# Performance work log

Hardware: AMD Instinct MI355X
Metric: run time of the kernel (lower is better)

The kernel has to match this reference:

```python
import jax, jax.numpy as jnp
import numpy as np

D_MODEL = 1024
N_HEADS = 16
D_H = D_MODEL // N_HEADS
MAX_LEN = 2048
BATCH = 2
SEQ = 2048
EPS = 1e-8
W_SCALE = 0.02


def _rms_norm(x, w):
    # RMSNorm: x * rsqrt(mean(x^2) + eps) * w
    ms = jnp.mean(jnp.square(x), axis=-1, keepdims=True)
    return w * (x * jax.lax.rsqrt(ms + EPS))


def setup_inputs() -> dict:
    key = jax.random.key(0)
    ks = jax.random.split(key, 12)
    d = D_MODEL
    inp = {
        "x": jax.random.normal(ks[0], (BATCH, SEQ, d), dtype=jnp.float32),
        "t_bias": jnp.zeros((1,), dtype=jnp.float32),  # unused by the module
        "p_bias": jax.random.normal(ks[1], (MAX_LEN, N_HEADS), dtype=jnp.float32),
        # AMS layer params (Linear stored as [in, out])
        "wq": jax.random.normal(ks[2], (d, d), dtype=jnp.float32) * W_SCALE,
        "bq": jnp.zeros((d,), dtype=jnp.float32),
        "wk": jax.random.normal(ks[3], (d, d), dtype=jnp.float32) * W_SCALE,
        "bk": jnp.zeros((d,), dtype=jnp.float32),
        "wv": jax.random.normal(ks[4], (d, d), dtype=jnp.float32) * W_SCALE,
        "bv": jnp.zeros((d,), dtype=jnp.float32),
        "wu": jax.random.normal(ks[5], (d, d), dtype=jnp.float32) * W_SCALE,
        "bu": jnp.zeros((d,), dtype=jnp.float32),
        "g_ams": jnp.ones((d,), dtype=jnp.float32),   # shared RMSNorm weight in AMSLayer
        # MFFN layer params
        "w0": jax.random.normal(ks[6], (d, d), dtype=jnp.float32) * W_SCALE,
        "b0": jnp.zeros((d,), dtype=jnp.float32),
        "w1": jax.random.normal(ks[7], (d, 2 * d), dtype=jnp.float32) * W_SCALE,
        "b1": jnp.zeros((2 * d,), dtype=jnp.float32),
        "w2": jax.random.normal(ks[8], (d, d), dtype=jnp.float32) * W_SCALE,
        "b2": jnp.zeros((d,), dtype=jnp.float32),
        "g_mffn": jnp.ones((d,), dtype=jnp.float32),
    }
    return inp


def reference(x, t_bias, p_bias, wq, bq, wk, bk, wv, bv, wu, bu, g_ams,
              w0, b0, w1, b1, w2, b2, g_mffn):
    B, S, d = x.shape
    H, dh = N_HEADS, D_H

    # ---- AMS layer ----
    x_norm = _rms_norm(x, g_ams)

    def proj(w, b):
        # [B,S,d] -> [B,H,S,dh]
        return (x_norm @ w + b).reshape(B, S, H, dh).transpose(0, 2, 1, 3)

    q = proj(wq, bq)
    k = proj(wk, bk)
    v = proj(wv, bv)

    scale = 1.0 / np.sqrt(dh).astype(np.float32)
    score = jnp.einsum('bhsd,bhtd->bhst', q, k) * scale
    # additive positional bias: p_bias[:S].T -> [H,S], broadcast over query dim
    score = score + p_bias[:S, :].T[None, :, None, :]

    attn = jax.nn.silu(score)                        # SiLU instead of softmax
    out = jnp.einsum('bhst,bhtd->bhsd', attn, v)
    out = out.transpose(0, 2, 1, 3).reshape(B, S, d)

    u = jax.nn.silu(x_norm @ wu + bu)
    ams_out = _rms_norm(out, g_ams) * u

    # ---- MFFN layer ----
    o = (ams_out @ w0 + b0) + x
    o_norm = _rms_norm(o, g_mffn)
    x12 = o_norm @ w1 + b1
    x1, x2 = jnp.split(x12, 2, axis=-1)
    swiglu = jax.nn.silu(x1) * x2
    return (swiglu @ w2 + b2) + o
```

## Files before the change

kernel.cpp:

```cpp
#include <hip/hip_runtime.h>
#include <stdint.h>
#include <math.h>


#define D    1024
#define NH   16
#define DH   64
#define B_   2
#define S_   2048
#define ROWS 4096
#define LQ   4096
#define EPSR 1e-8f

typedef unsigned short u16;
typedef __attribute__((ext_vector_type(8))) short short8;
typedef __attribute__((ext_vector_type(4))) float f32x4;

__device__ __forceinline__ float bf2f(u16 u) {
    union { uint32_t i; float f; } c; c.i = ((uint32_t)u) << 16; return c.f;
}
__device__ __forceinline__ u16 f2bf(float f) {
    union { float f; uint32_t i; } c; c.f = f;
    uint32_t x = c.i;
    x += 0x7fffu + ((x >> 16) & 1u);
    return (u16)(x >> 16);
}
__device__ __forceinline__ uint32_t pack2bf(float a, float b) {
    union { float f; uint32_t i; } ca, cb; ca.f = a; cb.f = b;
    return __builtin_amdgcn_perm(cb.i + 0x8000u, ca.i + 0x8000u, 0x07060302);
}
#define LOG2E 1.44269504f
__device__ __forceinline__ float silu_fast(float v) {
    return v * __builtin_amdgcn_rcpf(1.0f + __builtin_amdgcn_exp2f(v * -LOG2E));
}

__global__ __launch_bounds__(256) void transpose_all_kernel(
    const float* __restrict__ wq, const float* __restrict__ wk,
    const float* __restrict__ wv, const float* __restrict__ wu,
    const float* __restrict__ w0, const float* __restrict__ w2,
    const float* __restrict__ w1,
    u16* __restrict__ wT4, u16* __restrict__ w0T,
    u16* __restrict__ w2T, u16* __restrict__ w1T)
{
    const unsigned MI = 1u << 20;
    const int z = blockIdx.z;
    const float* W; u16* WT; int N; int noff = 0;
    switch (z) {
        case 0: W = wq; WT = wT4;          N = 1024; break;
        case 1: W = wk; WT = wT4 + 1 * MI; N = 1024; break;
        case 2: W = wv; WT = wT4 + 2 * MI; N = 1024; break;
        case 3: W = wu; WT = wT4 + 3 * MI; N = 1024; break;
        case 4: W = w0; WT = w0T;          N = 1024; break;
        case 5: W = w2; WT = w2T;          N = 1024; break;
        case 6: W = w1; WT = w1T;          N = 2048; noff = 0;    break;
        default:W = w1; WT = w1T;          N = 2048; noff = 1024; break;
    }
    __shared__ float T[64][65];
    const int tid = threadIdx.x;
    const int n0 = (blockIdx.x << 6) + noff;
    const int k0 = blockIdx.y << 6;
    const int rr = tid >> 4;
    const int cc = (tid & 15) << 2;
#pragma unroll
    for (int l = 0; l < 4; ++l) {
        const int r = rr + (l << 4);
        float4 v = *(const float4*)&W[(size_t)(k0 + r) * N + n0 + cc];
        T[cc + 0][r] = v.x; T[cc + 1][r] = v.y;
        T[cc + 2][r] = v.z; T[cc + 3][r] = v.w;
    }
    __syncthreads();
    const int n  = tid >> 2;
    const int ks = (tid & 3) << 4;
#pragma unroll
    for (int m = 0; m < 4; ++m) {
        const int k = ks + (m << 2);
        float4 v = *(const float4*)&T[n][k];
        ushort4 o;
        o.x = f2bf(v.x); o.y = f2bf(v.y); o.z = f2bf(v.z); o.w = f2bf(v.w);
        *(ushort4*)&WT[(size_t)(n0 + n) * 1024 + k0 + k] = o;
    }
}

__global__ __launch_bounds__(256) void pbt_kernel(
    const float* __restrict__ pb, float* __restrict__ pbT)
{
    const int tid = threadIdx.x;
    const int r = (blockIdx.x << 7) + (tid >> 1);
    const int c0 = (tid & 1) << 3;
    float4 v0 = *(const float4*)&pb[(size_t)r * NH + c0];
    float4 v1 = *(const float4*)&pb[(size_t)r * NH + c0 + 4];
    pbT[(size_t)(c0 + 0) * S_ + r] = v0.x;
    pbT[(size_t)(c0 + 1) * S_ + r] = v0.y;
    pbT[(size_t)(c0 + 2) * S_ + r] = v0.z;
    pbT[(size_t)(c0 + 3) * S_ + r] = v0.w;
    pbT[(size_t)(c0 + 4) * S_ + r] = v1.x;
    pbT[(size_t)(c0 + 5) * S_ + r] = v1.y;
    pbT[(size_t)(c0 + 6) * S_ + r] = v1.z;
    pbT[(size_t)(c0 + 7) * S_ + r] = v1.w;
}

__global__ __launch_bounds__(256) void rmsnorm_kernel(
    const float* __restrict__ inf, const u16* __restrict__ inb, int ldi,
    const float* __restrict__ g,
    const u16* __restrict__ mul, int ldm,
    u16* __restrict__ out, int ldo)
{
    const int row = blockIdx.x;
    const int tid = threadIdx.x;
    const int c = tid << 2;
    float x0, x1, x2, x3;
    if (inb) {
        ushort4 xi = *(const ushort4*)&inb[(size_t)row * ldi + c];
        x0 = bf2f(xi.x); x1 = bf2f(xi.y); x2 = bf2f(xi.z); x3 = bf2f(xi.w);
    } else {
        float4 xi = *(const float4*)&inf[(size_t)row * ldi + c];
        x0 = xi.x; x1 = xi.y; x2 = xi.z; x3 = xi.w;
    }
    float ss = x0*x0 + x1*x1 + x2*x2 + x3*x3;
#pragma unroll
    for (int off = 32; off > 0; off >>= 1) ss += __shfl_down(ss, off, 64);
    __shared__ float red[4];
    if ((tid & 63) == 0) red[tid >> 6] = ss;
    __syncthreads();
    float r = rsqrtf((red[0] + red[1] + red[2] + red[3]) * (1.0f / D) + EPSR);
    float4 gv = *(const float4*)&g[c];
    float v0 = x0 * r * gv.x, v1 = x1 * r * gv.y, v2 = x2 * r * gv.z, v3 = x3 * r * gv.w;
    if (mul) {
        ushort4 mi = *(const ushort4*)&mul[(size_t)row * ldm + c];
        v0 *= bf2f(mi.x); v1 *= bf2f(mi.y); v2 *= bf2f(mi.z); v3 *= bf2f(mi.w);
    }
    ushort4 o;
    o.x = f2bf(v0); o.y = f2bf(v1); o.z = f2bf(v2); o.w = f2bf(v3);
    *(ushort4*)&out[(size_t)row * ldo + c] = o;
}

__global__ __launch_bounds__(256) void gemm128(
    const u16* __restrict__ A, const u16* __restrict__ WT,
    const float* __restrict__ bs0, const float* __restrict__ bs1,
    const float* __restrict__ bs2, const float* __restrict__ bs3,
    u16* __restrict__ outb, int ldo, int actmask,
    u16* __restrict__ VT, int vtsel)
{
    __shared__ u16 As[128 * 32];
    __shared__ u16 Bs[128 * 32];
    const int tid  = threadIdx.x;
    const int wave = tid >> 6;
    const int lane = tid & 63;
    const int lm   = lane & 15;
    const int quad = lane >> 4;
    const int row0 = blockIdx.y << 7;
    const int col0 = blockIdx.x << 7;
    const int wr = (wave >> 1) << 6;
    const int wc = (wave & 1) << 6;

    const int srow = wave * 32 + (lane >> 2);
    const int skp  = (lane & 3) << 3;
    const u16* Ag = A  + (size_t)(row0 + srow) * 1024 + skp;
    const u16* Bg = WT + (size_t)(col0 + srow) * 1024 + skp;
    u16* Asd0 = &As[(wave * 32) * 32];
    u16* Asd1 = &As[(wave * 32 + 16) * 32];
    u16* Bsd0 = &Bs[(wave * 32) * 32];
    u16* Bsd1 = &Bs[(wave * 32 + 16) * 32];

    f32x4 acc[4][4] = {};

    for (int k0 = 0; k0 < 1024; k0 += 32) {
        __syncthreads();
        __builtin_amdgcn_global_load_lds(
            (const __attribute__((address_space(1))) void*)(Ag + k0),
            (__attribute__((address_space(3))) void*)Asd0, 16, 0, 0);
        __builtin_amdgcn_global_load_lds(
            (const __attribute__((address_space(1))) void*)(Ag + 16 * 1024 + k0),
            (__attribute__((address_space(3))) void*)Asd1, 16, 0, 0);
        __builtin_amdgcn_global_load_lds(
            (const __attribute__((address_space(1))) void*)(Bg + k0),
            (__attribute__((address_space(3))) void*)Bsd0, 16, 0, 0);
        __builtin_amdgcn_global_load_lds(
            (const __attribute__((address_space(1))) void*)(Bg + 16 * 1024 + k0),
            (__attribute__((address_space(3))) void*)Bsd1, 16, 0, 0);
        __syncthreads();
        short8 af[4], bf[4];
#pragma unroll
        for (int i = 0; i < 4; ++i)
            af[i] = *(const short8*)&As[(wr + i * 16 + lm) * 32 + quad * 8];
#pragma unroll
        for (int j = 0; j < 4; ++j)
            bf[j] = *(const short8*)&Bs[(wc + j * 16 + lm) * 32 + quad * 8];
#pragma unroll
        for (int i = 0; i < 4; ++i)
#pragma unroll
            for (int j = 0; j < 4; ++j)
                acc[i][j] = __builtin_amdgcn_mfma_f32_16x16x32_bf16(af[i], bf[j], acc[i][j], 0, 0, 0);
    }
    const int sel = col0 >> 10;
    const float* bias = (sel == 0) ? bs0 : (sel == 1) ? bs1 : (sel == 2) ? bs2 : bs3;
    const int act = (actmask >> sel) & 1;
    if (VT && sel == vtsel) {
        const int b = row0 >> 11;
#pragma unroll
        for (int j = 0; j < 4; ++j) {
            const int c2 = (col0 + wc + j * 16 + lm) & 1023;
            const int h  = c2 >> 6;
            const int dh = c2 & 63;
            const float bj = bias[c2];
            u16* vrow = VT + ((size_t)(b * NH + h) * 64 + dh) * (size_t)S_;
#pragma unroll
            for (int i = 0; i < 4; ++i) {
                const int tb = (row0 & 2047) + wr + i * 16 + quad * 4;
                ushort4 o;
                o.x = f2bf(acc[i][j][0] + bj);
                o.y = f2bf(acc[i][j][1] + bj);
                o.z = f2bf(acc[i][j][2] + bj);
                o.w = f2bf(acc[i][j][3] + bj);
                *(ushort4*)&vrow[tb] = o;
            }
        }
    } else {
#pragma unroll
        for (int j = 0; j < 4; ++j) {
            const int colg = col0 + wc + j * 16 + lm;
            const float bj = bias[colg & 1023];
#pragma unroll
            for (int i = 0; i < 4; ++i) {
#pragma unroll
                for (int r = 0; r < 4; ++r) {
                    const int rowg = row0 + wr + i * 16 + quad * 4 + r;
                    float v = acc[i][j][r] + bj;
                    if (act) v = silu_fast(v);
                    outb[(size_t)rowg * ldo + colg] = f2bf(v);
                }
            }
        }
    }
}

__global__ __launch_bounds__(256) void gemm64(
    const u16* __restrict__ A, int lda, const u16* __restrict__ WT,
    const float* __restrict__ bias,
    const float* __restrict__ res,
    float* __restrict__ outf, int ldo)
{
    __shared__ u16 As[128 * 32];
    __shared__ u16 Bs[64 * 32];
    const int tid  = threadIdx.x;
    const int wave = tid >> 6;
    const int lane = tid & 63;
    const int lm   = lane & 15;
    const int quad = lane >> 4;
    const int row0 = blockIdx.y << 7;
    const int col0 = blockIdx.x << 6;
    const int wr = (wave >> 1) << 6;
    const int wc = (wave & 1) << 5;

    const int srA = wave * 32 + (lane >> 2);
    const int srB = wave * 16 + (lane >> 2);
    const int skp = (lane & 3) << 3;
    const u16* Ag = A  + (size_t)(row0 + srA) * lda + skp;
    const u16* Bg = WT + (size_t)(col0 + srB) * 1024 + skp;
    u16* Asd0 = &As[(wave * 32) * 32];
    u16* Asd1 = &As[(wave * 32 + 16) * 32];
    u16* Bsd  = &Bs[(wave * 16) * 32];

    f32x4 acc[4][2] = {};

    for (int k0 = 0; k0 < 1024; k0 += 32) {
        __syncthreads();
        __builtin_amdgcn_global_load_lds(
            (const __attribute__((address_space(1))) void*)(Ag + k0),
            (__attribute__((address_space(3))) void*)Asd0, 16, 0, 0);
        __builtin_amdgcn_global_load_lds(
            (const __attribute__((address_space(1))) void*)(Ag + (size_t)16 * lda + k0),
            (__attribute__((address_space(3))) void*)Asd1, 16, 0, 0);
        __builtin_amdgcn_global_load_lds(
            (const __attribute__((address_space(1))) void*)(Bg + k0),
            (__attribute__((address_space(3))) void*)Bsd, 16, 0, 0);
        __syncthreads();
        short8 af[4], bf[2];
#pragma unroll
        for (int i = 0; i < 4; ++i)
            af[i] = *(const short8*)&As[(wr + i * 16 + lm) * 32 + quad * 8];
#pragma unroll
        for (int j = 0; j < 2; ++j)
            bf[j] = *(const short8*)&Bs[(wc + j * 16 + lm) * 32 + quad * 8];
#pragma unroll
        for (int i = 0; i < 4; ++i)
#pragma unroll
            for (int j = 0; j < 2; ++j)
                acc[i][j] = __builtin_amdgcn_mfma_f32_16x16x32_bf16(af[i], bf[j], acc[i][j], 0, 0, 0);
    }
#pragma unroll
    for (int j = 0; j < 2; ++j) {
        const int colg = col0 + wc + j * 16 + lm;
        const float bj = bias[colg];
#pragma unroll
        for (int i = 0; i < 4; ++i) {
#pragma unroll
            for (int r = 0; r < 4; ++r) {
                const int rowg = row0 + wr + i * 16 + quad * 4 + r;
                const size_t idx = (size_t)rowg * ldo + colg;
                float v = acc[i][j][r] + bj;
                if (res) v += res[idx];
                outf[idx] = v;
            }
        }
    }
}

__global__ __launch_bounds__(256, 4) void attn_mfma(
    const u16* __restrict__ qkvu, const u16* __restrict__ VT,
    const float* __restrict__ pbT, u16* __restrict__ out)
{
    __shared__ u16 Ks[2][64 * 64];
    __shared__ u16 Vs[2][64 * 64];
    const int tid  = threadIdx.x;
    const int wave = tid >> 6;
    const int lane = tid & 63;
    const int lm   = lane & 15;
    const int quad = lane >> 4;
    const int flat = blockIdx.x + (blockIdx.y << 5) + (blockIdx.z << 9);
    const int work = ((flat & 7) << 7) + (flat >> 3);
    const int s0 = (work & 31) << 6;
    const int h  = (work >> 5) & 15;
    const int b  = work >> 9;
    const size_t base = (size_t)b * S_ * LQ + (size_t)h * DH;
    const u16* q  = qkvu + base;
    const u16* kg = qkvu + base + 1024;
    const u16* vt = VT + (size_t)(b * NH + h) * 64 * S_;
    const float* pbh = pbT + (size_t)h * S_;

    short8 qf[2];
#pragma unroll
    for (int kk = 0; kk < 2; ++kk)
        qf[kk] = *(const short8*)&q[(size_t)(s0 + wave * 16 + lm) * LQ + kk * 32 + quad * 8];

    const int lr  = lane >> 3;
    const int gch = (lane & 7) ^ lr;
    const u16* kg0 = kg + (size_t)(16 * wave + lr) * LQ + gch * 8;
    const u16* vg0 = vt + (size_t)(16 * wave + lr) * S_ + gch * 8;
    const int cof0 = ((0 * 4 + quad) ^ (lm & 7)) * 8;
    const int cof1 = ((1 * 4 + quad) ^ (lm & 7)) * 8;
    const int a0   = (lm + ((quad & 1) << 5)) << 2;
    const bool hi  = quad >= 2;

#define GLDS(gp, lp) __builtin_amdgcn_global_load_lds( \
        (const __attribute__((address_space(1))) void*)(gp), \
        (__attribute__((address_space(3))) void*)(lp), 16, 0, 0)

    GLDS(kg0,                     &Ks[0][(16 * wave) * 64]);
    GLDS(kg0 + (size_t)8 * LQ,    &Ks[0][(16 * wave + 8) * 64]);
    GLDS(vg0,                     &Vs[0][(16 * wave) * 64]);
    GLDS(vg0 + (size_t)8 * S_,    &Vs[0][(16 * wave + 8) * 64]);

    f32x4 accO[4] = {};
    __syncthreads();

    for (int t0 = 0; t0 < S_; t0 += 64) {
        const int ib = (t0 >> 6) & 1;
        const int nb = ib ^ 1;
        float4 pbv[4];
#pragma unroll
        for (int mt = 0; mt < 4; ++mt)
            pbv[mt] = *(const float4*)&pbh[t0 + mt * 16 + quad * 4];
        if (t0 + 64 < S_) {
            const size_t tn = (size_t)(t0 + 64);
            GLDS(kg0 + tn * LQ,             &Ks[nb][(16 * wave) * 64]);
            GLDS(kg0 + (tn + 8) * LQ,       &Ks[nb][(16 * wave + 8) * 64]);
            GLDS(vg0 + tn,                  &Vs[nb][(16 * wave) * 64]);
            GLDS(vg0 + tn + (size_t)8 * S_, &Vs[nb][(16 * wave + 8) * 64]);
        }
        short8 kf[4][2];
#pragma unroll
        for (int mt = 0; mt < 4; ++mt) {
            kf[mt][0] = *(const short8*)&Ks[ib][(mt * 16 + lm) * 64 + cof0];
            kf[mt][1] = *(const short8*)&Ks[ib][(mt * 16 + lm) * 64 + cof1];
        }
        f32x4 st[4] = {};
#pragma unroll
        for (int mt = 0; mt < 4; ++mt)
#pragma unroll
            for (int kk = 0; kk < 2; ++kk)
                st[mt] = __builtin_amdgcn_mfma_f32_16x16x32_bf16(kf[mt][kk], qf[kk], st[mt], 0, 0, 0);
        int stp[4][2];
#pragma unroll
        for (int mt = 0; mt < 4; ++mt) {
            const float pbr[4] = {pbv[mt].x, pbv[mt].y, pbv[mt].z, pbv[mt].w};
            float p[4];
#pragma unroll
            for (int r = 0; r < 4; ++r) {
                const float a = fmaf(st[mt][r], 0.125f, pbr[r]);
                const float e = __builtin_amdgcn_exp2f(a * -LOG2E);
                p[r] = a * __builtin_amdgcn_rcpf(1.0f + e);
            }
            stp[mt][0] = (int)pack2bf(p[0], p[1]);
            stp[mt][1] = (int)pack2bf(p[2], p[3]);
        }
        short8 pf[2];
#pragma unroll
        for (int kk = 0; kk < 2; ++kk) {
            const int e0 = stp[2 * kk][0],     e1 = stp[2 * kk][1];
            const int o0 = stp[2 * kk + 1][0], o1 = stp[2 * kk + 1][1];
            const int w0a = __builtin_amdgcn_ds_bpermute(a0,      e0);
            const int w0b = __builtin_amdgcn_ds_bpermute(a0,      o0);
            const int w1a = __builtin_amdgcn_ds_bpermute(a0,      e1);
            const int w1b = __builtin_amdgcn_ds_bpermute(a0,      o1);
            const int w2a = __builtin_amdgcn_ds_bpermute(a0 + 64, e0);
            const int w2b = __builtin_amdgcn_ds_bpermute(a0 + 64, o0);
            const int w3a = __builtin_amdgcn_ds_bpermute(a0 + 64, e1);
            const int w3b = __builtin_amdgcn_ds_bpermute(a0 + 64, o1);
            int4 pw;
            pw.x = hi ? w0b : w0a;
            pw.y = hi ? w1b : w1a;
            pw.z = hi ? w2b : w2a;
            pw.w = hi ? w3b : w3a;
            pf[kk] = *(const short8*)&pw;
        }
        short8 vf[4][2];
#pragma unroll
        for (int nj = 0; nj < 4; ++nj) {
            vf[nj][0] = *(const short8*)&Vs[ib][(nj * 16 + lm) * 64 + cof0];
            vf[nj][1] = *(const short8*)&Vs[ib][(nj * 16 + lm) * 64 + cof1];
        }
#pragma unroll
        for (int nj = 0; nj < 4; ++nj)
#pragma unroll
            for (int kk = 0; kk < 2; ++kk)
                accO[nj] = __builtin_amdgcn_mfma_f32_16x16x32_bf16(pf[kk], vf[nj][kk], accO[nj], 0, 0, 0);
        __syncthreads();
    }
#undef GLDS
    const int srow = s0 + wave * 16 + quad * 4;
#pragma unroll
    for (int nj = 0; nj < 4; ++nj)
#pragma unroll
        for (int r = 0; r < 4; ++r)
            out[base + (size_t)(srow + r) * LQ + nj * 16 + lm] = f2bf(accO[nj][r]);
}

__global__ __launch_bounds__(256) void swiglu_kernel(u16* __restrict__ qkvu)
{
    const size_t e = ((size_t)blockIdx.x * 256 + threadIdx.x) << 2;
    const size_t r = e >> 10;
    const int    c = (int)(e & 1023);
    ushort4 a = *(const ushort4*)&qkvu[r * LQ + c];
    ushort4 b = *(const ushort4*)&qkvu[r * LQ + 1024 + c];
    ushort4 o;
    o.x = f2bf(silu_fast(bf2f(a.x)) * bf2f(b.x));
    o.y = f2bf(silu_fast(bf2f(a.y)) * bf2f(b.y));
    o.z = f2bf(silu_fast(bf2f(a.z)) * bf2f(b.z));
    o.w = f2bf(silu_fast(bf2f(a.w)) * bf2f(b.w));
    *(ushort4*)&qkvu[r * LQ + 2048 + c] = o;
}

extern "C" void kernel_launch(void* const* d_in, const int* in_sizes, int n_in,
                              void* d_out, int out_size, void* d_ws, size_t ws_size,
                              hipStream_t stream)
{
    const float* x      = (const float*)d_in[0];
    const float* pb     = (const float*)d_in[2];
    const float* wq     = (const float*)d_in[3];
    const float* bq     = (const float*)d_in[4];
    const float* wk     = (const float*)d_in[5];
    const float* bk     = (const float*)d_in[6];
    const float* wv     = (const float*)d_in[7];
    const float* bv     = (const float*)d_in[8];
    const float* wu     = (const float*)d_in[9];
    const float* bu     = (const float*)d_in[10];
    const float* g_ams  = (const float*)d_in[11];
    const float* w0     = (const float*)d_in[12];
    const float* b0     = (const float*)d_in[13];
    const float* w1     = (const float*)d_in[14];
    const float* b1     = (const float*)d_in[15];
    const float* w2     = (const float*)d_in[16];
    const float* b2     = (const float*)d_in[17];
    const float* g_mffn = (const float*)d_in[18];
    float* OUT = (float*)d_out;
    u16*   VT  = (u16*)d_out;
    float* pbT = (float*)((u16*)d_out + 4 * (1u << 20));

    const size_t MI = 1024 * 1024;
    u16* WS   = (u16*)d_ws;
    u16* wT4  = WS;
    u16* w0T  = WS + 4 * MI;
    u16* w2T  = WS + 5 * MI;
    u16* w1T  = WS + 6 * MI;
    u16* A0   = WS + 8 * MI;
    u16* QKVU = WS + 12 * MI;

    dim3 blk(256);

    transpose_all_kernel<<<dim3(16, 16, 8), blk, 0, stream>>>(
        wq, wk, wv, wu, w0, w2, w1, wT4, w0T, w2T, w1T);
    pbt_kernel<<<16, blk, 0, stream>>>(pb, pbT);

    rmsnorm_kernel<<<ROWS, blk, 0, stream>>>(x, nullptr, D, g_ams, nullptr, 0, A0, D);
    gemm128<<<dim3(32, 32), blk, 0, stream>>>(A0, wT4, bq, bk, bv, bu,
                                              QKVU, LQ, 0b1000, VT, 2);
    attn_mfma<<<dim3(32, 16, 2), blk, 0, stream>>>(QKVU, VT, pbT, QKVU);
    rmsnorm_kernel<<<ROWS, blk, 0, stream>>>(nullptr, QKVU, LQ, g_ams, QKVU + 3072, LQ, A0, D);
    gemm64<<<dim3(16, 32), blk, 0, stream>>>(A0, D, w0T, b0, x, OUT, D);
    rmsnorm_kernel<<<ROWS, blk, 0, stream>>>(OUT, nullptr, D, g_mffn, nullptr, 0, A0, D);
    gemm128<<<dim3(16, 32), blk, 0, stream>>>(A0, w1T, b1, b1 + 1024, b1, b1,
                                              QKVU, LQ, 0, nullptr, -1);
    swiglu_kernel<<<ROWS * D / 1024, blk, 0, stream>>>(QKVU);
    gemm64<<<dim3(16, 32), blk, 0, stream>>>(QKVU + 2048, LQ, w2T, b2, OUT, OUT, D);
    (void)ws_size; (void)in_sizes; (void)n_in; (void)out_size;
}
```

Measured before the change: 352.9 us.

## Rewrite attention with 32x32x16 MFMA, 128-row query tiles and permlane swap

The attention kernel moves from 16x16x32 to 32x32x16 bf16 MFMA tiles, with each wave owning 32 query rows and each block 128 rows, which halves the grid. The score-to-operand shuffle now uses v_permlane32_swap instead of eight ds_bpermute calls, packing uses v_cvt_pk_bf16_f32, and the positional bias is staged once into LDS rather than loaded from global every iteration. s_setprio hints are placed around the MFMA sections. The aim is to cut LDS and permute traffic and raise MFMA efficiency, at the cost of more accumulator registers per thread and fewer blocks, which may reduce occupancy.

New measurement: 343.8 us. 2.6% less time.

```diff
diff --git a/kernel.cpp b/kernel.cpp
--- a/kernel.cpp
+++ b/kernel.cpp
@@ -15,6 +15,8 @@
 typedef unsigned short u16;
 typedef __attribute__((ext_vector_type(8))) short short8;
 typedef __attribute__((ext_vector_type(4))) float f32x4;
+typedef __attribute__((ext_vector_type(16))) float f32x16;
+typedef __attribute__((ext_vector_type(4))) int int4v;
 
 __device__ __forceinline__ float bf2f(u16 u) {
     union { uint32_t i; float f; } c; c.i = ((uint32_t)u) << 16; return c.f;
@@ -24,10 +26,6 @@
     uint32_t x = c.i;
     x += 0x7fffu + ((x >> 16) & 1u);
     return (u16)(x >> 16);
-}
-__device__ __forceinline__ uint32_t pack2bf(float a, float b) {
-    union { float f; uint32_t i; } ca, cb; ca.f = a; cb.f = b;
-    return __builtin_amdgcn_perm(cb.i + 0x8000u, ca.i + 0x8000u, 0x07060302);
 }
 #define LOG2E 1.44269504f
 __device__ __forceinline__ float silu_fast(float v) {
@@ -312,35 +310,37 @@
 {
     __shared__ u16 Ks[2][64 * 64];
     __shared__ u16 Vs[2][64 * 64];
+    __shared__ float pbl[S_];
     const int tid  = threadIdx.x;
     const int wave = tid >> 6;
     const int lane = tid & 63;
-    const int lm   = lane & 15;
-    const int quad = lane >> 4;
-    const int flat = blockIdx.x + (blockIdx.y << 5) + (blockIdx.z << 9);
-    const int work = ((flat & 7) << 7) + (flat >> 3);
-    const int s0 = (work & 31) << 6;
-    const int h  = (work >> 5) & 15;
-    const int b  = work >> 9;
+    const int l31  = lane & 31;
+    const int hi   = lane >> 5;
+    const int l7   = lane & 7;
+    const int flat = blockIdx.x + (blockIdx.y << 4) + (blockIdx.z << 8);
+    const int work = ((flat & 7) << 6) + (flat >> 3);
+    const int s0 = (work & 15) << 7;
+    const int h  = (work >> 4) & 15;
+    const int b  = work >> 8;
     const size_t base = (size_t)b * S_ * LQ + (size_t)h * DH;
     const u16* q  = qkvu + base;
     const u16* kg = qkvu + base + 1024;
     const u16* vt = VT + (size_t)(b * NH + h) * 64 * S_;
     const float* pbh = pbT + (size_t)h * S_;
 
-    short8 qf[2];
-#pragma unroll
-    for (int kk = 0; kk < 2; ++kk)
-        qf[kk] = *(const short8*)&q[(size_t)(s0 + wave * 16 + lm) * LQ + kk * 32 + quad * 8];
+    for (int i = tid * 4; i < S_; i += 1024)
+        *(float4*)&pbl[i] = *(const float4*)&pbh[i];
+
+    const int qrow = s0 + wave * 32 + l31;
+    short8 qf[4];
+#pragma unroll
+    for (int i = 0; i < 4; ++i)
+        qf[i] = *(const short8*)&q[(size_t)qrow * LQ + i * 16 + hi * 8];
 
     const int lr  = lane >> 3;
-    const int gch = (lane & 7) ^ lr;
+    const int gch = l7 ^ lr;
     const u16* kg0 = kg + (size_t)(16 * wave + lr) * LQ + gch * 8;
     const u16* vg0 = vt + (size_t)(16 * wave + lr) * S_ + gch * 8;
-    const int cof0 = ((0 * 4 + quad) ^ (lm & 7)) * 8;
-    const int cof1 = ((1 * 4 + quad) ^ (lm & 7)) * 8;
-    const int a0   = (lm + ((quad & 1) << 5)) << 2;
-    const bool hi  = quad >= 2;
 
 #define GLDS(gp, lp) __builtin_amdgcn_global_load_lds( \
         (const __attribute__((address_space(1))) void*)(gp), \
@@ -351,16 +351,12 @@
     GLDS(vg0,                     &Vs[0][(16 * wave) * 64]);
     GLDS(vg0 + (size_t)8 * S_,    &Vs[0][(16 * wave + 8) * 64]);
 
-    f32x4 accO[4] = {};
+    f32x16 accO[2] = {};
     __syncthreads();
 
     for (int t0 = 0; t0 < S_; t0 += 64) {
         const int ib = (t0 >> 6) & 1;
         const int nb = ib ^ 1;
-        float4 pbv[4];
-#pragma unroll
-        for (int mt = 0; mt < 4; ++mt)
-            pbv[mt] = *(const float4*)&pbh[t0 + mt * 16 + quad * 4];
         if (t0 + 64 < S_) {
             const size_t tn = (size_t)(t0 + 64);
             GLDS(kg0 + tn * LQ,             &Ks[nb][(16 * wave) * 64]);
@@ -368,72 +364,57 @@
             GLDS(vg0 + tn,                  &Vs[nb][(16 * wave) * 64]);
             GLDS(vg0 + tn + (size_t)8 * S_, &Vs[nb][(16 * wave + 8) * 64]);
         }
-        short8 kf[4][2];
-#pragma unroll
-        for (int mt = 0; mt < 4; ++mt) {
-            kf[mt][0] = *(const short8*)&Ks[ib][(mt * 16 + lm) * 64 + cof0];
-            kf[mt][1] = *(const short8*)&Ks[ib][(mt * 16 + lm) * 64 + cof1];
-        }
-        f32x4 st[4] = {};
-#pragma unroll
-        for (int mt = 0; mt < 4; ++mt)
-#pragma unroll
-            for (int kk = 0; kk < 2; ++kk)
-                st[mt] = __builtin_amdgcn_mfma_f32_16x16x32_bf16(kf[mt][kk], qf[kk], st[mt], 0, 0, 0);
-        int stp[4][2];
-#pragma unroll
-        for (int mt = 0; mt < 4; ++mt) {
-            const float pbr[4] = {pbv[mt].x, pbv[mt].y, pbv[mt].z, pbv[mt].w};
-            float p[4];
-#pragma unroll
-            for (int r = 0; r < 4; ++r) {
-                const float a = fmaf(st[mt][r], 0.125f, pbr[r]);
-                const float e = __builtin_amdgcn_exp2f(a * -LOG2E);
-                p[r] = a * __builtin_amdgcn_rcpf(1.0f + e);
-            }
-            stp[mt][0] = (int)pack2bf(p[0], p[1]);
-            stp[mt][1] = (int)pack2bf(p[2], p[3]);
-        }
-        short8 pf[2];
-#pragma unroll
-        for (int kk = 0; kk < 2; ++kk) {
-            const int e0 = stp[2 * kk][0],     e1 = stp[2 * kk][1];
-            const int o0 = stp[2 * kk + 1][0], o1 = stp[2 * kk + 1][1];
-            const int w0a = __builtin_amdgcn_ds_bpermute(a0,      e0);
-            const int w0b = __builtin_amdgcn_ds_bpermute(a0,      o0);
-            const int w1a = __builtin_amdgcn_ds_bpermute(a0,      e1);
-            const int w1b = __builtin_amdgcn_ds_bpermute(a0,      o1);
-            const int w2a = __builtin_amdgcn_ds_bpermute(a0 + 64, e0);
-            const int w2b = __builtin_amdgcn_ds_bpermute(a0 + 64, o0);
-            const int w3a = __builtin_amdgcn_ds_bpermute(a0 + 64, e1);
-            const int w3b = __builtin_amdgcn_ds_bpermute(a0 + 64, o1);
-            int4 pw;
-            pw.x = hi ? w0b : w0a;
-            pw.y = hi ? w1b : w1a;
-            pw.z = hi ? w2b : w2a;
-            pw.w = hi ? w3b : w3a;
-            pf[kk] = *(const short8*)&pw;
-        }
-        short8 vf[4][2];
-#pragma unroll
-        for (int nj = 0; nj < 4; ++nj) {
-            vf[nj][0] = *(const short8*)&Vs[ib][(nj * 16 + lm) * 64 + cof0];
-            vf[nj][1] = *(const short8*)&Vs[ib][(nj * 16 + lm) * 64 + cof1];
-        }
-#pragma unroll
-        for (int nj = 0; nj < 4; ++nj)
-#pragma unroll
-            for (int kk = 0; kk < 2; ++kk)
-                accO[nj] = __builtin_amdgcn_mfma_f32_16x16x32_bf16(pf[kk], vf[nj][kk], accO[nj], 0, 0, 0);
+#pragma unroll
+        for (int half = 0; half < 2; ++half) {
+            const int ts = half << 5;
+            f32x16 st = {};
+            __builtin_amdgcn_s_setprio(1);
+#pragma unroll
+            for (int i = 0; i < 4; ++i) {
+                short8 kf = *(const short8*)&Ks[ib][(ts + l31) * 64 + (((2 * i + hi) ^ l7) << 3)];
+                st = __builtin_amdgcn_mfma_f32_32x32x16_bf16(kf, qf[i], st, 0, 0, 0);
+            }
+            __builtin_amdgcn_s_setprio(0);
+            int pk[8];
+#pragma unroll
+            for (int g = 0; g < 4; ++g) {
+                float4 pbv = *(const float4*)&pbl[t0 + ts + 8 * g + 4 * hi];
+                float p0 = silu_fast(fmaf(st[4 * g + 0], 0.125f, pbv.x));
+                float p1 = silu_fast(fmaf(st[4 * g + 1], 0.125f, pbv.y));
+                float p2 = silu_fast(fmaf(st[4 * g + 2], 0.125f, pbv.z));
+                float p3 = silu_fast(fmaf(st[4 * g + 3], 0.125f, pbv.w));
+                asm("v_cvt_pk_bf16_f32 %0, %1, %2" : "=v"(pk[2 * g])     : "v"(p0), "v"(p1));
+                asm("v_cvt_pk_bf16_f32 %0, %1, %2" : "=v"(pk[2 * g + 1]) : "v"(p2), "v"(p3));
+            }
+#pragma unroll
+            for (int m = 0; m < 2; ++m) {
+                int w0 = pk[4 * m + 0], w2 = pk[4 * m + 2];
+                int w1 = pk[4 * m + 1], w3 = pk[4 * m + 3];
+                asm("v_permlane32_swap_b32 %0, %1" : "+v"(w0), "+v"(w2));
+                asm("v_permlane32_swap_b32 %0, %1" : "+v"(w1), "+v"(w3));
+                union { int4v i; short8 s; } pa;
+                pa.i.x = w0; pa.i.y = w1; pa.i.z = w2; pa.i.w = w3;
+                __builtin_amdgcn_s_setprio(1);
+#pragma unroll
+                for (int n = 0; n < 2; ++n) {
+                    short8 vf = *(const short8*)&Vs[ib][(32 * n + l31) * 64 +
+                        ((((ts >> 3) + 2 * m + hi) ^ l7) << 3)];
+                    accO[n] = __builtin_amdgcn_mfma_f32_32x32x16_bf16(pa.s, vf, accO[n], 0, 0, 0);
+                }
+                __builtin_amdgcn_s_setprio(0);
+            }
+        }
         __syncthreads();
     }
 #undef GLDS
-    const int srow = s0 + wave * 16 + quad * 4;
-#pragma unroll
-    for (int nj = 0; nj < 4; ++nj)
-#pragma unroll
-        for (int r = 0; r < 4; ++r)
-            out[base + (size_t)(srow + r) * LQ + nj * 16 + lm] = f2bf(accO[nj][r]);
+    const int qb = s0 + wave * 32 + 4 * hi;
+#pragma unroll
+    for (int n = 0; n < 2; ++n)
+#pragma unroll
+        for (int r = 0; r < 16; ++r) {
+            const int qq = qb + (r & 3) + 8 * (r >> 2);
+            out[base + (size_t)qq * LQ + 32 * n + l31] = f2bf(accO[n][r]);
+        }
 }
 
 __global__ __launch_bounds__(256) void swiglu_kernel(u16* __restrict__ qkvu)
@@ -495,7 +476,7 @@
     rmsnorm_kernel<<<ROWS, blk, 0, stream>>>(x, nullptr, D, g_ams, nullptr, 0, A0, D);
     gemm128<<<dim3(32, 32), blk, 0, stream>>>(A0, wT4, bq, bk, bv, bu,
                                               QKVU, LQ, 0b1000, VT, 2);
-    attn_mfma<<<dim3(32, 16, 2), blk, 0, stream>>>(QKVU, VT, pbT, QKVU);
+    attn_mfma<<<dim3(16, 16, 2), blk, 0, stream>>>(QKVU, VT, pbT, QKVU);
     rmsnorm_kernel<<<ROWS, blk, 0, stream>>>(nullptr, QKVU, LQ, g_ams, QKVU + 3072, LQ, A0, D);
     gemm64<<<dim3(16, 32), blk, 0, stream>>>(A0, D, w0T, b0, x, OUT, D);
     rmsnorm_kernel<<<ROWS, blk, 0, stream>>>(OUT, nullptr, D, g_mffn, nullptr, 0, A0, D);
```
